# Optimization experiments

Hardware: AMD Instinct MI355X
Metric: run time of the kernel (lower is better)

Reference implementation:

```python
import jax, jax.numpy as jnp
import numpy as np

C_GMS = 0.0026  # constant c in the GMS map


def _median3(x):
    # 3x3 median with zero padding (matches kornia MedianBlur: conv2d-unfold
    # with zero padding, then median of the 9 values; odd count so torch's
    # lower-median == true median). x: [B,1,H,W]
    B, C, H, W = x.shape
    xp = jnp.pad(x, ((0, 0), (0, 0), (1, 1), (1, 1)))
    patches = jnp.stack(
        [xp[:, :, i:i + H, j:j + W] for i in range(3) for j in range(3)], axis=0
    )  # [9,B,1,H,W]
    return jnp.median(patches, axis=0)


def _prewitt(x):
    # fixed 2-channel Prewitt conv, VALID padding, then gradient magnitude
    Gx = jnp.array([[-1., 0., 1.], [-1., 0., 1.], [-1., 0., 1.]], dtype=x.dtype) / 3.0
    Gy = jnp.array([[1., 1., 1.], [0., 0., 0.], [-1., -1., -1.]], dtype=x.dtype) / 3.0
    k = jnp.stack([Gx, Gy])[:, None]  # [2,1,3,3] OIHW
    g = jax.lax.conv_general_dilated(
        x, k, window_strides=(1, 1), padding='VALID',
        dimension_numbers=('NCHW', 'OIHW', 'NCHW'))  # [B,2,H-2,W-2]
    return jnp.sqrt(jnp.sum(g * g, axis=1, keepdims=True))


def _gms_loss(Ii, Ir):
    x = jnp.mean(Ii, axis=1, keepdims=True)  # channel mean -> grayscale
    y = jnp.mean(Ir, axis=1, keepdims=True)
    gI = _prewitt(_median3(x))
    gR = _prewitt(_median3(y))
    gmap = (2.0 * gI * gR + C_GMS) / (gI * gI + gR * gR + C_GMS)
    return jnp.mean(1.0 - gmap)


def _avg_pool2(x):
    # avg_pool2d(kernel=2, stride=2)
    B, C, H, W = x.shape
    return x.reshape(B, C, H // 2, 2, W // 2, 2).mean(axis=(3, 5))


def setup_inputs() -> dict:
    key = jax.random.key(0)
    k1, k2 = jax.random.split(key)
    Ii = jax.random.uniform(k1, (16, 3, 512, 512), dtype=jnp.float32)
    Ir = jax.random.uniform(k2, (16, 3, 512, 512), dtype=jnp.float32)
    return {"Ii": Ii, "Ir": Ir}


def reference(Ii, Ir):
    total = _gms_loss(Ii, Ir)
    for _ in range(3):  # fixed 4-scale pyramid
        Ii = _avg_pool2(Ii)
        Ir = _avg_pool2(Ir)
        total = total + _gms_loss(Ii, Ir)
    return total / 4.0
```

## Files before the change

kernel.cpp:

```cpp
#include <hip/hip_runtime.h>

#define C_GMS 0.0026f

__device__ __forceinline__ float dppL(float x) {
    return __int_as_float(__builtin_amdgcn_mov_dpp(__float_as_int(x), 0x138, 0xf, 0xf, true));
}
__device__ __forceinline__ float dppR(float x) {
    return __int_as_float(__builtin_amdgcn_mov_dpp(__float_as_int(x), 0x130, 0xf, 0xf, true));
}
__device__ __forceinline__ float med3f(float a, float b, float c) {
    return __builtin_amdgcn_fmed3f(a, b, c);
}

#define N0 2560
#define N1 2560
#define N2 768
#define N3 256
#define NTOT 6144

template<int TRIP, class LoadFn, class PoolFn>
__device__ __forceinline__ float gms_core(int lane, int Hk, int R0, int iend, int c,
                                          int phalf, LoadFn loadrow2, PoolFn dopool)
{
    auto medrow = [&](float ga, float gb, float gc, float& m, float& rs) {
        float lo = fminf(fminf(ga, gb), gc);
        float me = med3f(ga, gb, gc);
        float hi = fmaxf(fmaxf(ga, gb), gc);
        float lmax = fmaxf(fmaxf(dppL(lo), lo), dppR(lo));
        float mid  = med3f(dppL(me), me, dppR(me));
        float hmin = fminf(fminf(dppL(hi), hi), dppR(hi));
        m  = med3f(lmax, mid, hmin);
        rs = m + dppL(m) + dppR(m);
    };

    float xa, ya, xb, yb, xc, yc, xd, yd, xe, ye;
    loadrow2(R0 - 1, xa, ya);
    loadrow2(R0,     xb, yb);
    loadrow2(R0 + 1, xc, yc);
    loadrow2(R0 + 2, xd, yd);
    loadrow2(R0 + 3, xe, ye);

    float n0x, n0y, n1x, n1y;
    loadrow2(R0 + 4, n0x, n0y);
    loadrow2(R0 + 5, n1x, n1y);

    float mx0, mx1, mx2, rx0, rx1, rx2;
    float my0, my1, my2, ry0, ry1, ry2;
    medrow(xa, xb, xc, mx0, rx0); medrow(ya, yb, yc, my0, ry0);
    dopool(xb, xc, yb, yc, phalf);
    medrow(xb, xc, xd, mx1, rx1); medrow(yb, yc, yd, my1, ry1);
    medrow(xc, xd, xe, mx2, rx2); medrow(yc, yd, ye, my2, ry2);

    float gx2 = xd, gx3 = xe, gy2 = yd, gy3 = ye;
    const bool outLane = (lane >= 2) && (lane <= 61) && (c <= Hk - 2);
    const float C9 = 9.0f * C_GMS;
    float acc = 0.0f;

    #pragma unroll
    for (int j = 0; j < TRIP; ++j) {
        const int i = R0 + j;
        float pfx, pfy;
        loadrow2(i + 6, pfx, pfy);

        float csx = mx0 + mx1 + mx2;
        float csy = my0 + my1 + my2;
        float Gxx = dppR(csx) - dppL(csx);
        float Gxy = dppR(csy) - dppL(csy);
        float Gyx = rx0 - rx2;
        float Gyy = ry0 - ry2;
        float a = fmaf(Gxx, Gxx, Gyx * Gyx);
        float b = fmaf(Gxy, Gxy, Gyy * Gyy);
        float t = a + b;
        float s = __builtin_amdgcn_sqrtf(a * b);
        float den = t + C9;
        float diff = fmaf(-2.0f, s, t);
        float r = __builtin_amdgcn_rcpf(den);
        if (outLane && (i < iend)) acc = fmaf(diff, r, acc);

        if (((i + 3) & 1) == 1) dopool(gx2, gx3, gy2, gy3, (i + 2) >> 1);

        float mxn, rxn, myn, ryn;
        medrow(gx2, gx3, n0x, mxn, rxn);
        medrow(gy2, gy3, n0y, myn, ryn);
        mx0 = mx1; mx1 = mx2; mx2 = mxn; rx0 = rx1; rx1 = rx2; rx2 = rxn;
        my0 = my1; my1 = my2; my2 = myn; ry0 = ry1; ry1 = ry2; ry2 = ryn;
        gx2 = gx3; gx3 = n0x; gy2 = gy3; gy3 = n0y;
        n0x = n1x; n0y = n1y; n1x = pfx; n1y = pfy;
    }

    for (int off = 32; off; off >>= 1) acc += __shfl_down(acc, off, 64);
    return acc;
}

__global__ __launch_bounds__(256) void msgms_scale0(
    const float* __restrict__ Ii, const float* __restrict__ Ir,
    float* __restrict__ X1, float* __restrict__ Y1, float* __restrict__ P)
{
    const int lane = threadIdx.x & 63;
    const int u = blockIdx.x * 4 + (threadIdx.x >> 6);
    const int s  = u % 5;
    const int t1 = u / 5;
    const int k  = t1 % 32;
    const int b  = t1 / 32;

    const int B  = 120 * s;
    const int c0 = B + 2 * lane;
    const int R0 = k * 16;
    const int iend = min(R0 + 16, 510);

    const float* PX = Ii + (size_t)b * 3 * 262144;
    const float* PY = Ir + (size_t)b * 3 * 262144;

    const int cc = min(c0, 510);
    const float cw = (c0 <= 511) ? (1.0f / 3.0f) : 0.0f;

    auto loadrow2 = [&](int r, float2& vx, float2& vy) {
        int rc = min(max(r, 0), 511);
        float m = (r == rc) ? cw : 0.0f;
        int o = rc * 512 + cc;
        float2 x0 = *(const float2*)(PX + o);
        float2 x1 = *(const float2*)(PX + o + 262144);
        float2 x2 = *(const float2*)(PX + o + 524288);
        float2 y0 = *(const float2*)(PY + o);
        float2 y1 = *(const float2*)(PY + o + 262144);
        float2 y2 = *(const float2*)(PY + o + 524288);
        vx.x = (x0.x + x1.x + x2.x) * m; vx.y = (x0.y + x1.y + x2.y) * m;
        vy.x = (y0.x + y1.x + y2.x) * m; vy.y = (y0.y + y1.y + y2.y) * m;
    };

    auto medrow = [&](float2 ga, float2 gb, float2 gc, float2& m, float2& rs) {
        float lo0 = fminf(fminf(ga.x, gb.x), gc.x);
        float lo1 = fminf(fminf(ga.y, gb.y), gc.y);
        float me0 = med3f(ga.x, gb.x, gc.x);
        float me1 = med3f(ga.y, gb.y, gc.y);
        float hi0 = fmaxf(fmaxf(ga.x, gb.x), gc.x);
        float hi1 = fmaxf(fmaxf(ga.y, gb.y), gc.y);
        float lmax0 = fmaxf(fmaxf(dppL(lo1), lo0), lo1);
        float lmax1 = fmaxf(fmaxf(lo0, lo1), dppR(lo0));
        float mid0  = med3f(dppL(me1), me0, me1);
        float mid1  = med3f(me0, me1, dppR(me0));
        float hmin0 = fminf(fminf(dppL(hi1), hi0), hi1);
        float hmin1 = fminf(fminf(hi0, hi1), dppR(hi0));
        m.x = med3f(lmax0, mid0, hmin0);
        m.y = med3f(lmax1, mid1, hmin1);
        float ms = m.x + m.y;
        rs.x = dppL(m.y) + ms;
        rs.y = ms + dppR(m.x);
    };

    const int ostart = (s == 0) ? 1 : (120 * s + 6);
    const int oend   = (s == 4) ? 510 : (120 * s + 125);
    const bool out0 = (c0 >= ostart)     && (c0 <= oend);
    const bool out1 = (c0 + 1 >= ostart) && (c0 + 1 <= oend);

    const int q = 60 * s + lane;
    const bool poolLane = (lane < ((s == 4) ? 16 : 60));
    const int phalf = R0 >> 1;
    const int pend  = min(phalf + 8, 256);
    auto dopool = [&](float2 bx, float2 cx, float2 by, float2 cy, int p) {
        if (p < phalf || p >= pend) return;
        if (poolLane) {
            size_t o = ((size_t)b * 256 + p) * 256 + q;
            X1[o] = ((bx.x + bx.y) + (cx.x + cx.y)) * 0.25f;
            Y1[o] = ((by.x + by.y) + (cy.x + cy.y)) * 0.25f;
        }
    };

    float2 xa, ya, xb, yb, xc, yc, xd, yd, xe, ye;
    loadrow2(R0 - 1, xa, ya);
    loadrow2(R0,     xb, yb);
    loadrow2(R0 + 1, xc, yc);
    loadrow2(R0 + 2, xd, yd);
    loadrow2(R0 + 3, xe, ye);

    float2 n0x, n0y, n1x, n1y;
    loadrow2(R0 + 4, n0x, n0y);
    loadrow2(R0 + 5, n1x, n1y);

    float2 mx0, mx1, mx2, rx0, rx1, rx2;
    float2 my0, my1, my2, ry0, ry1, ry2;
    medrow(xa, xb, xc, mx0, rx0); medrow(ya, yb, yc, my0, ry0);
    dopool(xb, xc, yb, yc, phalf);
    medrow(xb, xc, xd, mx1, rx1); medrow(yb, yc, yd, my1, ry1);
    medrow(xc, xd, xe, mx2, rx2); medrow(yc, yd, ye, my2, ry2);

    float2 gx2 = xd, gx3 = xe, gy2 = yd, gy3 = ye;
    const float C9 = 9.0f * C_GMS;
    float acc = 0.0f;

    #pragma unroll
    for (int j = 0; j < 16; ++j) {
        const int i = R0 + j;
        float2 pfx, pfy;
        loadrow2(i + 6, pfx, pfy);

        float2 csx, csy;
        csx.x = mx0.x + mx1.x + mx2.x; csx.y = mx0.y + mx1.y + mx2.y;
        csy.x = my0.x + my1.x + my2.x; csy.y = my0.y + my1.y + my2.y;
        float Gxx0 = csx.y - dppL(csx.y), Gxx1 = dppR(csx.x) - csx.x;
        float Gxy0 = csy.y - dppL(csy.y), Gxy1 = dppR(csy.x) - csy.x;
        float Gyx0 = rx0.x - rx2.x,       Gyx1 = rx0.y - rx2.y;
        float Gyy0 = ry0.x - ry2.x,       Gyy1 = ry0.y - ry2.y;

        float a0 = fmaf(Gxx0, Gxx0, Gyx0 * Gyx0);
        float b0 = fmaf(Gxy0, Gxy0, Gyy0 * Gyy0);
        float t0 = a0 + b0;
        float s0 = __builtin_amdgcn_sqrtf(a0 * b0);
        float d0 = fmaf(-2.0f, s0, t0);
        float r0 = __builtin_amdgcn_rcpf(t0 + C9);
        if (out0 && (i < iend)) acc = fmaf(d0, r0, acc);

        float a1 = fmaf(Gxx1, Gxx1, Gyx1 * Gyx1);
        float b1 = fmaf(Gxy1, Gxy1, Gyy1 * Gyy1);
        float t1v = a1 + b1;
        float s1 = __builtin_amdgcn_sqrtf(a1 * b1);
        float d1 = fmaf(-2.0f, s1, t1v);
        float r1 = __builtin_amdgcn_rcpf(t1v + C9);
        if (out1 && (i < iend)) acc = fmaf(d1, r1, acc);

        if (((i + 3) & 1) == 1) dopool(gx2, gx3, gy2, gy3, (i + 2) >> 1);

        float2 mxn, rxn, myn, ryn;
        medrow(gx2, gx3, n0x, mxn, rxn);
        medrow(gy2, gy3, n0y, myn, ryn);
        mx0 = mx1; mx1 = mx2; mx2 = mxn; rx0 = rx1; rx1 = rx2; rx2 = rxn;
        my0 = my1; my1 = my2; my2 = myn; ry0 = ry1; ry1 = ry2; ry2 = ryn;
        gx2 = gx3; gx3 = n0x; gy2 = gy3; gy3 = n0y;
        n0x = n1x; n0y = n1y; n1x = pfx; n1y = pfy;
    }

    for (int off = 32; off; off >>= 1) acc += __shfl_down(acc, off, 64);
    if (lane == 0) P[u] = acc;
}

template<int G>
__device__ __forceinline__ void phaseR(
    int u, const float* __restrict__ X1, const float* __restrict__ Y1,
    int nstrips, int nchunks, float* __restrict__ P)
{
    constexpr int Hk = 256 / G;
    const int lane = threadIdx.x & 63;
    const int s  = u % nstrips;
    const int t1 = u / nstrips;
    const int k  = t1 % nchunks;
    const int b  = t1 / nchunks;

    const int c  = 60 * s - 1 + lane;
    const int R0 = k * 8;
    const int iend = min(R0 + 8, Hk - 2);

    const float* Xp = X1 + (size_t)b * 65536;
    const float* Yp = Y1 + (size_t)b * 65536;

    const int cc = min(max(c, 0), Hk - 1);
    const float cval = ((c >= 0) && (c < Hk)) ? 1.0f : 0.0f;

    auto loadrow2 = [&](int r, float& vx, float& vy) {
        int rc = min(max(r, 0), Hk - 1);
        float m = (r == rc) ? cval : 0.0f;
        if constexpr (G == 1) {
            int o = rc * 256 + cc;
            vx = Xp[o] * m; vy = Yp[o] * m;
        } else if constexpr (G == 2) {
            int o = (rc * 2) * 256 + cc * 2;
            float2 a0 = *(const float2*)(Xp + o);
            float2 a1 = *(const float2*)(Xp + o + 256);
            float2 b0 = *(const float2*)(Yp + o);
            float2 b1 = *(const float2*)(Yp + o + 256);
            float q = 0.25f * m;
            vx = ((a0.x + a0.y) + (a1.x + a1.y)) * q;
            vy = ((b0.x + b0.y) + (b1.x + b1.y)) * q;
        } else {
            int o = (rc * 4) * 256 + cc * 4;
            float sx = 0.0f, sy = 0.0f;
            #pragma unroll
            for (int fr = 0; fr < 4; ++fr) {
                float4 t = *(const float4*)(Xp + o + fr * 256);
                float4 q = *(const float4*)(Yp + o + fr * 256);
                sx += (t.x + t.y) + (t.z + t.w);
                sy += (q.x + q.y) + (q.z + q.w);
            }
            float q = 0.0625f * m;
            vx = sx * q; vy = sy * q;
        }
    };
    auto nopool = [&](float, float, float, float, int) {};

    float acc = gms_core<8>(lane, Hk, R0, iend, c, 0, loadrow2, nopool);
    if (lane == 0) P[u] = acc;
}

__global__ __launch_bounds__(256) void msgms_rest(
    const float* __restrict__ X1, const float* __restrict__ Y1,
    float* __restrict__ P)
{
    const int u = blockIdx.x * 4 + (threadIdx.x >> 6);
    if      (u < N1)      phaseR<1>(u,           X1, Y1, 5, 32, P + N0);
    else if (u < N1 + N2) phaseR<2>(u - N1,      X1, Y1, 3, 16, P + N0 + N1);
    else                  phaseR<4>(u - N1 - N2, X1, Y1, 2,  8, P + N0 + N1 + N2);
}

__global__ __launch_bounds__(256) void msgms_final(
    const float* __restrict__ P, float* __restrict__ out)
{
    const int tid = threadIdx.x;
    const double w0 = 1.0 / (4.0 * 16.0 * 510.0 * 510.0);
    const double w1 = 1.0 / (4.0 * 16.0 * 254.0 * 254.0);
    const double w2 = 1.0 / (4.0 * 16.0 * 126.0 * 126.0);
    const double w3 = 1.0 / (4.0 * 16.0 * 62.0 * 62.0);
    double v = 0.0;
    for (int i = tid; i < NTOT; i += 256) {
        double w = (i < N0) ? w0 : (i < N0 + N1) ? w1 : (i < N0 + N1 + N2) ? w2 : w3;
        v += (double)P[i] * w;
    }
    for (int off = 32; off; off >>= 1) v += __shfl_down(v, off, 64);
    __shared__ double wsum[4];
    if ((tid & 63) == 0) wsum[tid >> 6] = v;
    __syncthreads();
    if (tid == 0) out[0] = (float)(wsum[0] + wsum[1] + wsum[2] + wsum[3]);
}

extern "C" void kernel_launch(void* const* d_in, const int* in_sizes, int n_in,
                              void* d_out, int out_size, void* d_ws, size_t ws_size,
                              hipStream_t stream) {
    const float* Ii = (const float*)d_in[0];
    const float* Ir = (const float*)d_in[1];
    float* out = (float*)d_out;

    char* ws = (char*)d_ws;
    float* P  = (float*)ws;
    float* X1 = P + NTOT;
    float* Y1 = X1 + 16 * 256 * 256;

    msgms_scale0<<<N0 / 4, 256, 0, stream>>>(Ii, Ir, X1, Y1, P);
    msgms_rest<<<(N1 + N2 + N3) / 4, 256, 0, stream>>>(X1, Y1, P);
    msgms_final<<<1, 256, 0, stream>>>(P, out);
}
```

Baseline: 144.5 us.

## Stage grayscale rows through LDS ring buffer shared across five waves in scale0

The scale-0 kernel now uses one 320-thread block per (batch, 16-row strip). Four waves cooperatively load each full 512-column row once, reduce the three channels to grayscale, and write it into an 8-slot shared-memory ring. All five waves then read their 128-column windows from LDS, which removes the redundant global loads caused by overlapping column halos (the stride drops from 120 to 96 columns per wave). The cost is a block barrier every row, a software-pipelined register prefetch, and an idle fifth wave during staging.

```diff
diff --git a/kernel.cpp b/kernel.cpp
--- a/kernel.cpp
+++ b/kernel.cpp
@@ -92,40 +92,79 @@
     return acc;
 }
 
-__global__ __launch_bounds__(256) void msgms_scale0(
+#define RC0 16
+
+__global__ __launch_bounds__(320) void msgms_scale0(
     const float* __restrict__ Ii, const float* __restrict__ Ir,
     float* __restrict__ X1, float* __restrict__ Y1, float* __restrict__ P)
 {
-    const int lane = threadIdx.x & 63;
-    const int u = blockIdx.x * 4 + (threadIdx.x >> 6);
-    const int s  = u % 5;
-    const int t1 = u / 5;
-    const int k  = t1 % 32;
-    const int b  = t1 / 32;
-
-    const int B  = 120 * s;
-    const int c0 = B + 2 * lane;
-    const int R0 = k * 16;
-    const int iend = min(R0 + 16, 510);
+    const int tid  = threadIdx.x;
+    const int lane = tid & 63;
+    const int w    = tid >> 6;
+    const int bid  = blockIdx.x;
+    const int b    = bid >> 5;
+    const int k    = bid & 31;
+    const int R0   = k * RC0;
+    const int iend = min(R0 + RC0, 510);
+    const int u    = bid * 5 + w;
 
     const float* PX = Ii + (size_t)b * 3 * 262144;
     const float* PY = Ir + (size_t)b * 3 * 262144;
 
-    const int cc = min(c0, 510);
-    const float cw = (c0 <= 511) ? (1.0f / 3.0f) : 0.0f;
+    __shared__ float gx[8][512];
+    __shared__ float gy[8][512];
+
+    const int  tc     = tid * 2;
+    const bool stager = (tid < 256);
+
+    auto issue6 = [&](int r, float2* L) {
+        if (stager) {
+            int rc = min(max(r, 0), 511);
+            size_t o = (size_t)rc * 512 + tc;
+            L[0] = *(const float2*)(PX + o);
+            L[1] = *(const float2*)(PX + o + 262144);
+            L[2] = *(const float2*)(PX + o + 524288);
+            L[3] = *(const float2*)(PY + o);
+            L[4] = *(const float2*)(PY + o + 262144);
+            L[5] = *(const float2*)(PY + o + 524288);
+        }
+    };
+    auto flush6 = [&](int r, float2* L) {
+        if (stager) {
+            int slot = r & 7;
+            float m = (r >= 0 && r < 512) ? (1.0f / 3.0f) : 0.0f;
+            float2 vx, vy;
+            vx.x = (L[0].x + L[1].x + L[2].x) * m;
+            vx.y = (L[0].y + L[1].y + L[2].y) * m;
+            vy.x = (L[3].x + L[4].x + L[5].x) * m;
+            vy.y = (L[3].y + L[4].y + L[5].y) * m;
+            *(float2*)&gx[slot][tc] = vx;
+            *(float2*)&gy[slot][tc] = vy;
+        }
+    };
+    auto bar = [&]() {
+        asm volatile("s_waitcnt lgkmcnt(0)" ::: "memory");
+        __builtin_amdgcn_s_barrier();
+        asm volatile("" ::: "memory");
+    };
+
+    float2 Lp[7][6];
+    #pragma unroll
+    for (int j = 0; j < 7; ++j) issue6(R0 - 1 + j, Lp[j]);
+    #pragma unroll
+    for (int j = 0; j < 7; ++j) flush6(R0 - 1 + j, Lp[j]);
+
+    float2 LQ[2][6];
+    issue6(min(R0 + 6, iend + 3), LQ[0]);
+    bar();
+
+    const int B  = 96 * w;
+    const int c0 = B + 2 * lane;
 
     auto loadrow2 = [&](int r, float2& vx, float2& vy) {
-        int rc = min(max(r, 0), 511);
-        float m = (r == rc) ? cw : 0.0f;
-        int o = rc * 512 + cc;
-        float2 x0 = *(const float2*)(PX + o);
-        float2 x1 = *(const float2*)(PX + o + 262144);
-        float2 x2 = *(const float2*)(PX + o + 524288);
-        float2 y0 = *(const float2*)(PY + o);
-        float2 y1 = *(const float2*)(PY + o + 262144);
-        float2 y2 = *(const float2*)(PY + o + 524288);
-        vx.x = (x0.x + x1.x + x2.x) * m; vx.y = (x0.y + x1.y + x2.y) * m;
-        vy.x = (y0.x + y1.x + y2.x) * m; vy.y = (y0.y + y1.y + y2.y) * m;
+        int slot = r & 7;
+        vx = *(const float2*)&gx[slot][c0];
+        vy = *(const float2*)&gy[slot][c0];
     };
 
     auto medrow = [&](float2 ga, float2 gb, float2 gc, float2& m, float2& rs) {
@@ -148,13 +187,15 @@
         rs.y = ms + dppR(m.x);
     };
 
-    const int ostart = (s == 0) ? 1 : (120 * s + 6);
-    const int oend   = (s == 4) ? 510 : (120 * s + 125);
+    const int ostart = (w == 0) ? 1   : (96 * w + 16);
+    const int oend   = (w == 4) ? 510 : (96 * w + 111);
     const bool out0 = (c0 >= ostart)     && (c0 <= oend);
     const bool out1 = (c0 + 1 >= ostart) && (c0 + 1 <= oend);
 
-    const int q = 60 * s + lane;
-    const bool poolLane = (lane < ((s == 4) ? 16 : 60));
+    const int q = 48 * w + lane;
+    const bool poolLane = (w == 0) ? (lane <= 55)
+                        : (w == 4) ? (lane >= 8)
+                                   : (lane >= 8 && lane <= 55);
     const int phalf = R0 >> 1;
     const int pend  = min(phalf + 8, 256);
     auto dopool = [&](float2 bx, float2 cx, float2 by, float2 cy, int p) {
@@ -172,7 +213,6 @@
     loadrow2(R0 + 1, xc, yc);
     loadrow2(R0 + 2, xd, yd);
     loadrow2(R0 + 3, xe, ye);
-
     float2 n0x, n0y, n1x, n1y;
     loadrow2(R0 + 4, n0x, n0y);
     loadrow2(R0 + 5, n1x, n1y);
@@ -189,10 +229,16 @@
     float acc = 0.0f;
 
     #pragma unroll
-    for (int j = 0; j < 16; ++j) {
+    for (int j = 0; j < RC0; ++j) {
         const int i = R0 + j;
+        const int r_this = min(i + 6, iend + 3);
+        const int r_next = min(i + 7, iend + 3);
+        issue6(r_next, LQ[(j + 1) & 1]);
+        flush6(r_this, LQ[j & 1]);
+        bar();
+
         float2 pfx, pfy;
-        loadrow2(i + 6, pfx, pfy);
+        loadrow2(r_this, pfx, pfy);
 
         float2 csx, csy;
         csx.x = mx0.x + mx1.x + mx2.x; csx.y = mx0.y + mx1.y + mx2.y;
@@ -267,21 +313,21 @@
             float2 a1 = *(const float2*)(Xp + o + 256);
             float2 b0 = *(const float2*)(Yp + o);
             float2 b1 = *(const float2*)(Yp + o + 256);
-            float q = 0.25f * m;
-            vx = ((a0.x + a0.y) + (a1.x + a1.y)) * q;
-            vy = ((b0.x + b0.y) + (b1.x + b1.y)) * q;
+            float qq = 0.25f * m;
+            vx = ((a0.x + a0.y) + (a1.x + a1.y)) * qq;
+            vy = ((b0.x + b0.y) + (b1.x + b1.y)) * qq;
         } else {
             int o = (rc * 4) * 256 + cc * 4;
             float sx = 0.0f, sy = 0.0f;
             #pragma unroll
             for (int fr = 0; fr < 4; ++fr) {
                 float4 t = *(const float4*)(Xp + o + fr * 256);
-                float4 q = *(const float4*)(Yp + o + fr * 256);
+                float4 qv = *(const float4*)(Yp + o + fr * 256);
                 sx += (t.x + t.y) + (t.z + t.w);
-                sy += (q.x + q.y) + (q.z + q.w);
+                sy += (qv.x + qv.y) + (qv.z + qv.w);
             }
-            float q = 0.0625f * m;
-            vx = sx * q; vy = sy * q;
+            float qq = 0.0625f * m;
+            vx = sx * qq; vy = sy * qq;
         }
     };
     auto nopool = [&](float, float, float, float, int) {};
@@ -332,7 +378,7 @@
     float* X1 = P + NTOT;
     float* Y1 = X1 + 16 * 256 * 256;
 
-    msgms_scale0<<<N0 / 4, 256, 0, stream>>>(Ii, Ir, X1, Y1, P);
+    msgms_scale0<<<512, 320, 0, stream>>>(Ii, Ir, X1, Y1, P);
     msgms_rest<<<(N1 + N2 + N3) / 4, 256, 0, stream>>>(X1, Y1, P);
     msgms_final<<<1, 256, 0, stream>>>(P, out);
 }
```

Measured after the change: 159.7 us. +10.5%, slower.

## Process two columns per lane at pyramid scales 1 and 2, skip surplus prefetch rows

Applied to the files above, without the earlier changes.

Pulls the two-column-per-lane scale-0 loop out into a shared templated core and reuses it for scales 1 and 2. Those scales drop from one column per lane to two (scale 1 uses 3 strips of 96 columns, scale 2 uses a single strip with float4 pooled loads), which cuts the wave count and the halo overlap between strips. Prefetch loads for rows past the chunk's last needed row are redirected to a zeroed out-of-range row. The trade-off is more live registers per lane and fewer waves in the second kernel, which may lower occupancy.

```diff
diff --git a/kernel.cpp b/kernel.cpp
--- a/kernel.cpp
+++ b/kernel.cpp
@@ -13,10 +13,10 @@
 }
 
 #define N0 2560
-#define N1 2560
-#define N2 768
+#define N1 1536
+#define N2 256
 #define N3 256
-#define NTOT 6144
+#define NTOT 4608
 
 template<int TRIP, class LoadFn, class PoolFn>
 __device__ __forceinline__ float gms_core(int lane, int Hk, int R0, int iend, int c,
@@ -60,7 +60,10 @@
     for (int j = 0; j < TRIP; ++j) {
         const int i = R0 + j;
         float pfx, pfy;
-        loadrow2(i + 6, pfx, pfy);
+        {
+            int rp = (i + 6 <= iend + 3) ? (i + 6) : -1;
+            loadrow2(rp, pfx, pfy);
+        }
 
         float csx = mx0 + mx1 + mx2;
         float csy = my0 + my1 + my2;
@@ -72,9 +75,8 @@
         float b = fmaf(Gxy, Gxy, Gyy * Gyy);
         float t = a + b;
         float s = __builtin_amdgcn_sqrtf(a * b);
-        float den = t + C9;
         float diff = fmaf(-2.0f, s, t);
-        float r = __builtin_amdgcn_rcpf(den);
+        float r = __builtin_amdgcn_rcpf(t + C9);
         if (outLane && (i < iend)) acc = fmaf(diff, r, acc);
 
         if (((i + 3) & 1) == 1) dopool(gx2, gx3, gy2, gy3, (i + 2) >> 1);
@@ -92,42 +94,10 @@
     return acc;
 }
 
-__global__ __launch_bounds__(256) void msgms_scale0(
-    const float* __restrict__ Ii, const float* __restrict__ Ir,
-    float* __restrict__ X1, float* __restrict__ Y1, float* __restrict__ P)
-{
-    const int lane = threadIdx.x & 63;
-    const int u = blockIdx.x * 4 + (threadIdx.x >> 6);
-    const int s  = u % 5;
-    const int t1 = u / 5;
-    const int k  = t1 % 32;
-    const int b  = t1 / 32;
-
-    const int B  = 120 * s;
-    const int c0 = B + 2 * lane;
-    const int R0 = k * 16;
-    const int iend = min(R0 + 16, 510);
-
-    const float* PX = Ii + (size_t)b * 3 * 262144;
-    const float* PY = Ir + (size_t)b * 3 * 262144;
-
-    const int cc = min(c0, 510);
-    const float cw = (c0 <= 511) ? (1.0f / 3.0f) : 0.0f;
-
-    auto loadrow2 = [&](int r, float2& vx, float2& vy) {
-        int rc = min(max(r, 0), 511);
-        float m = (r == rc) ? cw : 0.0f;
-        int o = rc * 512 + cc;
-        float2 x0 = *(const float2*)(PX + o);
-        float2 x1 = *(const float2*)(PX + o + 262144);
-        float2 x2 = *(const float2*)(PX + o + 524288);
-        float2 y0 = *(const float2*)(PY + o);
-        float2 y1 = *(const float2*)(PY + o + 262144);
-        float2 y2 = *(const float2*)(PY + o + 524288);
-        vx.x = (x0.x + x1.x + x2.x) * m; vx.y = (x0.y + x1.y + x2.y) * m;
-        vy.x = (y0.x + y1.x + y2.x) * m; vy.y = (y0.y + y1.y + y2.y) * m;
-    };
-
+template<int TRIP, class LoadFn, class PoolFn>
+__device__ __forceinline__ float gms_core2(int R0, int iend, bool out0, bool out1,
+                                           int phalf, LoadFn loadrow2, PoolFn dopool)
+{
     auto medrow = [&](float2 ga, float2 gb, float2 gc, float2& m, float2& rs) {
         float lo0 = fminf(fminf(ga.x, gb.x), gc.x);
         float lo1 = fminf(fminf(ga.y, gb.y), gc.y);
@@ -148,6 +118,112 @@
         rs.y = ms + dppR(m.x);
     };
 
+    float2 xa, ya, xb, yb, xc, yc, xd, yd, xe, ye;
+    loadrow2(R0 - 1, xa, ya);
+    loadrow2(R0,     xb, yb);
+    loadrow2(R0 + 1, xc, yc);
+    loadrow2(R0 + 2, xd, yd);
+    loadrow2(R0 + 3, xe, ye);
+
+    float2 n0x, n0y, n1x, n1y;
+    loadrow2(R0 + 4, n0x, n0y);
+    loadrow2(R0 + 5, n1x, n1y);
+
+    float2 mx0, mx1, mx2, rx0, rx1, rx2;
+    float2 my0, my1, my2, ry0, ry1, ry2;
+    medrow(xa, xb, xc, mx0, rx0); medrow(ya, yb, yc, my0, ry0);
+    dopool(xb, xc, yb, yc, phalf);
+    medrow(xb, xc, xd, mx1, rx1); medrow(yb, yc, yd, my1, ry1);
+    medrow(xc, xd, xe, mx2, rx2); medrow(yc, yd, ye, my2, ry2);
+
+    float2 gx2 = xd, gx3 = xe, gy2 = yd, gy3 = ye;
+    const float C9 = 9.0f * C_GMS;
+    float acc = 0.0f;
+
+    #pragma unroll
+    for (int j = 0; j < TRIP; ++j) {
+        const int i = R0 + j;
+        float2 pfx, pfy;
+        {
+            int rp = (i + 6 <= iend + 3) ? (i + 6) : -1;
+            loadrow2(rp, pfx, pfy);
+        }
+
+        float2 csx, csy;
+        csx.x = mx0.x + mx1.x + mx2.x; csx.y = mx0.y + mx1.y + mx2.y;
+        csy.x = my0.x + my1.x + my2.x; csy.y = my0.y + my1.y + my2.y;
+        float Gxx0 = csx.y - dppL(csx.y), Gxx1 = dppR(csx.x) - csx.x;
+        float Gxy0 = csy.y - dppL(csy.y), Gxy1 = dppR(csy.x) - csy.x;
+        float Gyx0 = rx0.x - rx2.x,       Gyx1 = rx0.y - rx2.y;
+        float Gyy0 = ry0.x - ry2.x,       Gyy1 = ry0.y - ry2.y;
+
+        float a0 = fmaf(Gxx0, Gxx0, Gyx0 * Gyx0);
+        float b0 = fmaf(Gxy0, Gxy0, Gyy0 * Gyy0);
+        float t0 = a0 + b0;
+        float s0 = __builtin_amdgcn_sqrtf(a0 * b0);
+        float d0 = fmaf(-2.0f, s0, t0);
+        float r0 = __builtin_amdgcn_rcpf(t0 + C9);
+        if (out0 && (i < iend)) acc = fmaf(d0, r0, acc);
+
+        float a1 = fmaf(Gxx1, Gxx1, Gyx1 * Gyx1);
+        float b1 = fmaf(Gxy1, Gxy1, Gyy1 * Gyy1);
+        float t1v = a1 + b1;
+        float s1 = __builtin_amdgcn_sqrtf(a1 * b1);
+        float d1 = fmaf(-2.0f, s1, t1v);
+        float r1 = __builtin_amdgcn_rcpf(t1v + C9);
+        if (out1 && (i < iend)) acc = fmaf(d1, r1, acc);
+
+        if (((i + 3) & 1) == 1) dopool(gx2, gx3, gy2, gy3, (i + 2) >> 1);
+
+        float2 mxn, rxn, myn, ryn;
+        medrow(gx2, gx3, n0x, mxn, rxn);
+        medrow(gy2, gy3, n0y, myn, ryn);
+        mx0 = mx1; mx1 = mx2; mx2 = mxn; rx0 = rx1; rx1 = rx2; rx2 = rxn;
+        my0 = my1; my1 = my2; my2 = myn; ry0 = ry1; ry1 = ry2; ry2 = ryn;
+        gx2 = gx3; gx3 = n0x; gy2 = gy3; gy3 = n0y;
+        n0x = n1x; n0y = n1y; n1x = pfx; n1y = pfy;
+    }
+
+    for (int off = 32; off; off >>= 1) acc += __shfl_down(acc, off, 64);
+    return acc;
+}
+
+__global__ __launch_bounds__(256) void msgms_scale0(
+    const float* __restrict__ Ii, const float* __restrict__ Ir,
+    float* __restrict__ X1, float* __restrict__ Y1, float* __restrict__ P)
+{
+    const int lane = threadIdx.x & 63;
+    const int u = blockIdx.x * 4 + (threadIdx.x >> 6);
+    const int s  = u % 5;
+    const int t1 = u / 5;
+    const int k  = t1 % 32;
+    const int b  = t1 / 32;
+
+    const int B  = 120 * s;
+    const int c0 = B + 2 * lane;
+    const int R0 = k * 16;
+    const int iend = min(R0 + 16, 510);
+
+    const float* PX = Ii + (size_t)b * 3 * 262144;
+    const float* PY = Ir + (size_t)b * 3 * 262144;
+
+    const int cc = min(c0, 510);
+    const float cw = (c0 <= 511) ? (1.0f / 3.0f) : 0.0f;
+
+    auto loadrow2 = [&](int r, float2& vx, float2& vy) {
+        int rc = min(max(r, 0), 511);
+        float m = (r == rc) ? cw : 0.0f;
+        int o = rc * 512 + cc;
+        float2 x0 = *(const float2*)(PX + o);
+        float2 x1 = *(const float2*)(PX + o + 262144);
+        float2 x2 = *(const float2*)(PX + o + 524288);
+        float2 y0 = *(const float2*)(PY + o);
+        float2 y1 = *(const float2*)(PY + o + 262144);
+        float2 y2 = *(const float2*)(PY + o + 524288);
+        vx.x = (x0.x + x1.x + x2.x) * m; vx.y = (x0.y + x1.y + x2.y) * m;
+        vy.x = (y0.x + y1.x + y2.x) * m; vy.y = (y0.y + y1.y + y2.y) * m;
+    };
+
     const int ostart = (s == 0) ? 1 : (120 * s + 6);
     const int oend   = (s == 4) ? 510 : (120 * s + 125);
     const bool out0 = (c0 >= ostart)     && (c0 <= oend);
@@ -166,84 +242,97 @@
         }
     };
 
-    float2 xa, ya, xb, yb, xc, yc, xd, yd, xe, ye;
-    loadrow2(R0 - 1, xa, ya);
-    loadrow2(R0,     xb, yb);
-    loadrow2(R0 + 1, xc, yc);
-    loadrow2(R0 + 2, xd, yd);
-    loadrow2(R0 + 3, xe, ye);
-
-    float2 n0x, n0y, n1x, n1y;
-    loadrow2(R0 + 4, n0x, n0y);
-    loadrow2(R0 + 5, n1x, n1y);
-
-    float2 mx0, mx1, mx2, rx0, rx1, rx2;
-    float2 my0, my1, my2, ry0, ry1, ry2;
-    medrow(xa, xb, xc, mx0, rx0); medrow(ya, yb, yc, my0, ry0);
-    dopool(xb, xc, yb, yc, phalf);
-    medrow(xb, xc, xd, mx1, rx1); medrow(yb, yc, yd, my1, ry1);
-    medrow(xc, xd, xe, mx2, rx2); medrow(yc, yd, ye, my2, ry2);
-
-    float2 gx2 = xd, gx3 = xe, gy2 = yd, gy3 = ye;
-    const float C9 = 9.0f * C_GMS;
-    float acc = 0.0f;
-
-    #pragma unroll
-    for (int j = 0; j < 16; ++j) {
-        const int i = R0 + j;
-        float2 pfx, pfy;
-        loadrow2(i + 6, pfx, pfy);
-
-        float2 csx, csy;
-        csx.x = mx0.x + mx1.x + mx2.x; csx.y = mx0.y + mx1.y + mx2.y;
-        csy.x = my0.x + my1.x + my2.x; csy.y = my0.y + my1.y + my2.y;
-        float Gxx0 = csx.y - dppL(csx.y), Gxx1 = dppR(csx.x) - csx.x;
-        float Gxy0 = csy.y - dppL(csy.y), Gxy1 = dppR(csy.x) - csy.x;
-        float Gyx0 = rx0.x - rx2.x,       Gyx1 = rx0.y - rx2.y;
-        float Gyy0 = ry0.x - ry2.x,       Gyy1 = ry0.y - ry2.y;
-
-        float a0 = fmaf(Gxx0, Gxx0, Gyx0 * Gyx0);
-        float b0 = fmaf(Gxy0, Gxy0, Gyy0 * Gyy0);
-        float t0 = a0 + b0;
-        float s0 = __builtin_amdgcn_sqrtf(a0 * b0);
-        float d0 = fmaf(-2.0f, s0, t0);
-        float r0 = __builtin_amdgcn_rcpf(t0 + C9);
-        if (out0 && (i < iend)) acc = fmaf(d0, r0, acc);
-
-        float a1 = fmaf(Gxx1, Gxx1, Gyx1 * Gyx1);
-        float b1 = fmaf(Gxy1, Gxy1, Gyy1 * Gyy1);
-        float t1v = a1 + b1;
-        float s1 = __builtin_amdgcn_sqrtf(a1 * b1);
-        float d1 = fmaf(-2.0f, s1, t1v);
-        float r1 = __builtin_amdgcn_rcpf(t1v + C9);
-        if (out1 && (i < iend)) acc = fmaf(d1, r1, acc);
-
-        if (((i + 3) & 1) == 1) dopool(gx2, gx3, gy2, gy3, (i + 2) >> 1);
-
-        float2 mxn, rxn, myn, ryn;
-        medrow(gx2, gx3, n0x, mxn, rxn);
-        medrow(gy2, gy3, n0y, myn, ryn);
-        mx0 = mx1; mx1 = mx2; mx2 = mxn; rx0 = rx1; rx1 = rx2; rx2 = rxn;
-        my0 = my1; my1 = my2; my2 = myn; ry0 = ry1; ry1 = ry2; ry2 = ryn;
-        gx2 = gx3; gx3 = n0x; gy2 = gy3; gy3 = n0y;
-        n0x = n1x; n0y = n1y; n1x = pfx; n1y = pfy;
-    }
-
-    for (int off = 32; off; off >>= 1) acc += __shfl_down(acc, off, 64);
+    float acc = gms_core2<16>(R0, iend, out0, out1, phalf, loadrow2, dopool);
     if (lane == 0) P[u] = acc;
 }
 
-template<int G>
-__device__ __forceinline__ void phaseR(
+__device__ __forceinline__ void phaseR1f2(
+    int v, const float* __restrict__ X1, const float* __restrict__ Y1,
+    float* __restrict__ P)
+{
+    const int lane = threadIdx.x & 63;
+    const int s  = v % 3;
+    const int t1 = v / 3;
+    const int k  = t1 % 32;
+    const int b  = t1 / 32;
+
+    const int c0 = 96 * s + 2 * lane;
+    const int R0 = k * 8;
+    const int iend = min(R0 + 8, 254);
+
+    const float* Xp = X1 + (size_t)b * 65536;
+    const float* Yp = Y1 + (size_t)b * 65536;
+
+    const int cc = min(c0, 254);
+    const float cw = (c0 <= 254) ? 1.0f : 0.0f;
+
+    auto loadrow2 = [&](int r, float2& vx, float2& vy) {
+        int rc = min(max(r, 0), 255);
+        float m = (r == rc) ? cw : 0.0f;
+        int o = rc * 256 + cc;
+        float2 ax = *(const float2*)(Xp + o);
+        float2 ay = *(const float2*)(Yp + o);
+        vx.x = ax.x * m; vx.y = ax.y * m;
+        vy.x = ay.x * m; vy.y = ay.y * m;
+    };
+    auto nopool = [&](float2, float2, float2, float2, int) {};
+
+    const int ostart = (s == 0) ? 1   : (96 * s + 8);
+    const int oend   = (s == 2) ? 254 : (96 * s + 103);
+    const bool out0 = (c0 >= ostart)     && (c0 <= oend);
+    const bool out1 = (c0 + 1 >= ostart) && (c0 + 1 <= oend);
+
+    float acc = gms_core2<8>(R0, iend, out0, out1, 0, loadrow2, nopool);
+    if (lane == 0) P[v] = acc;
+}
+
+__device__ __forceinline__ void phaseR2f2(
+    int v, const float* __restrict__ X1, const float* __restrict__ Y1,
+    float* __restrict__ P)
+{
+    const int lane = threadIdx.x & 63;
+    const int k  = v % 16;
+    const int b  = v / 16;
+
+    const int c0 = 2 * lane;
+    const int R0 = k * 8;
+    const int iend = min(R0 + 8, 126);
+
+    const float* Xp = X1 + (size_t)b * 65536;
+    const float* Yp = Y1 + (size_t)b * 65536;
+
+    auto loadrow2 = [&](int r, float2& vx, float2& vy) {
+        int rc = min(max(r, 0), 127);
+        float m = (r == rc) ? 0.25f : 0.0f;
+        int o = (rc * 2) * 256 + 4 * lane;
+        float4 a0 = *(const float4*)(Xp + o);
+        float4 a1 = *(const float4*)(Xp + o + 256);
+        float4 b0 = *(const float4*)(Yp + o);
+        float4 b1 = *(const float4*)(Yp + o + 256);
+        vx.x = ((a0.x + a0.y) + (a1.x + a1.y)) * m;
+        vx.y = ((a0.z + a0.w) + (a1.z + a1.w)) * m;
+        vy.x = ((b0.x + b0.y) + (b1.x + b1.y)) * m;
+        vy.y = ((b0.z + b0.w) + (b1.z + b1.w)) * m;
+    };
+    auto nopool = [&](float2, float2, float2, float2, int) {};
+
+    const bool out0 = (c0 >= 1) && (c0 <= 126);
+    const bool out1 = (c0 + 1 >= 1) && (c0 + 1 <= 126);
+
+    float acc = gms_core2<8>(R0, iend, out0, out1, 0, loadrow2, nopool);
+    if (lane == 0) P[v] = acc;
+}
+
+__device__ __forceinline__ void phaseR4(
     int u, const float* __restrict__ X1, const float* __restrict__ Y1,
-    int nstrips, int nchunks, float* __restrict__ P)
-{
-    constexpr int Hk = 256 / G;
+    float* __restrict__ P)
+{
+    constexpr int Hk = 64;
     const int lane = threadIdx.x & 63;
-    const int s  = u % nstrips;
-    const int t1 = u / nstrips;
-    const int k  = t1 % nchunks;
-    const int b  = t1 / nchunks;
+    const int s  = u % 2;
+    const int t1 = u / 2;
+    const int k  = t1 % 8;
+    const int b  = t1 / 8;
 
     const int c  = 60 * s - 1 + lane;
     const int R0 = k * 8;
@@ -258,31 +347,17 @@
     auto loadrow2 = [&](int r, float& vx, float& vy) {
         int rc = min(max(r, 0), Hk - 1);
         float m = (r == rc) ? cval : 0.0f;
-        if constexpr (G == 1) {
-            int o = rc * 256 + cc;
-            vx = Xp[o] * m; vy = Yp[o] * m;
-        } else if constexpr (G == 2) {
-            int o = (rc * 2) * 256 + cc * 2;
-            float2 a0 = *(const float2*)(Xp + o);
-            float2 a1 = *(const float2*)(Xp + o + 256);
-            float2 b0 = *(const float2*)(Yp + o);
-            float2 b1 = *(const float2*)(Yp + o + 256);
-            float q = 0.25f * m;
-            vx = ((a0.x + a0.y) + (a1.x + a1.y)) * q;
-            vy = ((b0.x + b0.y) + (b1.x + b1.y)) * q;
-        } else {
-            int o = (rc * 4) * 256 + cc * 4;
-            float sx = 0.0f, sy = 0.0f;
-            #pragma unroll
-            for (int fr = 0; fr < 4; ++fr) {
-                float4 t = *(const float4*)(Xp + o + fr * 256);
-                float4 q = *(const float4*)(Yp + o + fr * 256);
-                sx += (t.x + t.y) + (t.z + t.w);
-                sy += (q.x + q.y) + (q.z + q.w);
-            }
-            float q = 0.0625f * m;
-            vx = sx * q; vy = sy * q;
+        int o = (rc * 4) * 256 + cc * 4;
+        float sx = 0.0f, sy = 0.0f;
+        #pragma unroll
+        for (int fr = 0; fr < 4; ++fr) {
+            float4 t = *(const float4*)(Xp + o + fr * 256);
+            float4 qv = *(const float4*)(Yp + o + fr * 256);
+            sx += (t.x + t.y) + (t.z + t.w);
+            sy += (qv.x + qv.y) + (qv.z + qv.w);
         }
+        float qq = 0.0625f * m;
+        vx = sx * qq; vy = sy * qq;
     };
     auto nopool = [&](float, float, float, float, int) {};
 
@@ -295,9 +370,9 @@
     float* __restrict__ P)
 {
     const int u = blockIdx.x * 4 + (threadIdx.x >> 6);
-    if      (u < N1)      phaseR<1>(u,           X1, Y1, 5, 32, P + N0);
-    else if (u < N1 + N2) phaseR<2>(u - N1,      X1, Y1, 3, 16, P + N0 + N1);
-    else                  phaseR<4>(u - N1 - N2, X1, Y1, 2,  8, P + N0 + N1 + N2);
+    if      (u < N1)      phaseR1f2(u,           X1, Y1, P + N0);
+    else if (u < N1 + N2) phaseR2f2(u - N1,      X1, Y1, P + N0 + N1);
+    else                  phaseR4 (u - N1 - N2,  X1, Y1, P + N0 + N1 + N2);
 }
 
 __global__ __launch_bounds__(256) void msgms_final(
```

Measured after the change: 140.2 us. 1.03x faster.
